# Kernel optimization log

Measured on AMD Instinct MI355X. Metric: run time of the kernel, lower is better.

## Reference

```python
import jax, jax.numpy as jnp
import numpy as np

N = 10000        # nodes
E = 160000       # edges
C = 128          # channel multiplicity (128x0e input)
RBF = 20         # edge_attr_dim
HID = 32         # edge MLP hidden
WN = 3 * C       # tp.weight_numel: 3 uvu paths (0e x Y_l -> l), 128 weights each


def setup_inputs() -> dict:
    key = jax.random.key(0)
    ks = jax.random.split(key, 12)
    f = lambda k, s, sc=1.0: jax.random.normal(k, s, jnp.float32) * sc
    return {
        "node_feat": f(ks[0], (N, C)),
        "edge_attr": f(ks[1], (E, RBF)),
        "edge_rsh": f(ks[2], (E, 9)),
        "edge_index": jax.random.randint(ks[3], (2, E), 0, N),
        # mlp_edge_scalar: Linear(2C->32), Linear(32->WN)
        "Ws1": f(ks[4], (2 * C, HID), 1.0 / np.sqrt(2 * C)), "bs1": jnp.zeros((HID,), jnp.float32),
        "Ws2": f(ks[5], (HID, WN), 1.0 / np.sqrt(HID)), "bs2": jnp.zeros((WN,), jnp.float32),
        # mlp_edge_rbf: Linear(20->32), Linear(32->WN)
        "Wr1": f(ks[6], (RBF, HID), 1.0 / np.sqrt(RBF)), "br1": jnp.zeros((HID,), jnp.float32),
        "Wr2": f(ks[7], (HID, WN), 1.0 / np.sqrt(HID)), "br2": jnp.zeros((WN,), jnp.float32),
        "lin2_w0": f(ks[8], (C, C)), "lin2_b0": jnp.zeros((C,), jnp.float32),
        "lin2_w1": f(ks[9], (C, C)),
        "lin2_w2": f(ks[10], (C, C)),
    }


def reference(node_feat, edge_attr, edge_rsh, edge_index,
              Ws1, bs1, Ws2, bs2, Wr1, br1, Wr2, br2,
              lin2_w0, lin2_b0, lin2_w1, lin2_w2):
    src, dst = edge_index[0], edge_index[1]
    xi = node_feat[src]            # [E, C] gathered scalars (center node)
    xj = node_feat[dst]            # [E, C] gathered scalars (neighbor)

    # First-layer branch: inner_dot of pure scalars -> elementwise product;
    # slice [:, C:] is empty, so s0 = concat(x_i scalars, x_j scalars).
    s0 = jnp.concatenate([xi, xj], axis=-1)  # [E, 2C]

    silu = jax.nn.silu
    w_s = silu(s0 @ Ws1 + bs1) @ Ws2 + bs2            # [E, 3C]
    w_r = silu(edge_attr @ Wr1 + br1) @ Wr2 + br2      # [E, 3C]
    tpw = w_s * w_r                                    # gated tensor-product weights

    w0, w1, w2 = tpw[:, :C], tpw[:, C:2 * C], tpw[:, 2 * C:]
    y0, y1, y2 = edge_rsh[:, :1], edge_rsh[:, 1:4], edge_rsh[:, 4:9]

    # uvu tensor product: per edge, per channel u: w_l[u] * x[u] * Y_l[m]
    m0 = (w0 * xj) * y0                                        # [E, C]
    m1 = (w1 * xj)[:, :, None] * y1[:, None, :]                # [E, C, 3]
    m2 = (w2 * xj)[:, :, None] * y2[:, None, :]                # [E, C, 5]
    msg = jnp.concatenate(
        [m0, m1.reshape(-1, 3 * C), m2.reshape(-1, 5 * C)], axis=-1)  # [E, 9C]

    # scatter-add to destination (edge_index[0])
    accu = jax.ops.segment_sum(msg, src, num_segments=node_feat.shape[0])  # [N, 9C]

    # lin_node2: equivariant linear (per-l channel mixing, bias on scalars only)
    a0 = accu[:, :C]
    a1 = accu[:, C:4 * C].reshape(-1, C, 3)
    a2 = accu[:, 4 * C:].reshape(-1, C, 5)
    inv = 1.0 / np.sqrt(C)  # e3nn o3.Linear fan-in normalization
    o0 = a0 @ lin2_w0 * inv + lin2_b0
    o1 = jnp.einsum('ncm,cd->ndm', a1, lin2_w1) * inv
    o2 = jnp.einsum('ncm,cd->ndm', a2, lin2_w2) * inv
    return jnp.concatenate([o0, o1.reshape(-1, 3 * C), o2.reshape(-1, 5 * C)], axis=-1)
```

## Files before the change

### kernel.cpp

```cpp
#include <hip/hip_runtime.h>
#include <hip/hip_bf16.h>
#include <math.h>

#define NN   10000
#define EE   160000
#define CC   128
#define RBFD 20
#define HIDD 32
#define WND  384
#define MROW 1152
#define EPB  64

typedef _Float16 half2_t __attribute__((ext_vector_type(2)));

__device__ __forceinline__ half2_t u2h(unsigned int u)
{
    union { unsigned int u; half2_t h; } c; c.u = u; return c.h;
}
__device__ __forceinline__ unsigned int pack_h2(float a, float b)
{
    union { half2_t h; unsigned int u; } c;
    c.h.x = (_Float16)a; c.h.y = (_Float16)b; return c.u;
}

__device__ __align__(16) float g_proj[(size_t)NN * 64];
__device__ __align__(16) float g_accu[(size_t)NN * MROW];
__device__ int g_deg[NN];
__device__ int g_offs[NN + 1];
__device__ int g_rel[EE];
__device__ int g_ord[EE];

__device__ __forceinline__ float silu_f(float x) { return x / (1.f + __expf(-x)); }

__global__ __launch_bounds__(256) void zero_kernel()
{
    int tid = blockIdx.x * 256 + threadIdx.x;
    if (tid < NN) g_deg[tid] = 0;
    float4* p = reinterpret_cast<float4*>(g_accu);
    float4 z = make_float4(0.f, 0.f, 0.f, 0.f);
    int n4 = NN * MROW / 4;
    for (int i = tid; i < n4; i += gridDim.x * 256) p[i] = z;
}

__global__ __launch_bounds__(256) void hist_kernel(const int* __restrict__ edge_index)
{
    int e = blockIdx.x * 256 + threadIdx.x;
    if (e < EE) g_rel[e] = atomicAdd(&g_deg[edge_index[e]], 1);
}

__global__ __launch_bounds__(256) void scan_kernel()
{
    __shared__ int sP[256];
    int t = threadIdx.x;
    int lo = t * 40, hi = min(lo + 40, NN);
    int sum = 0;
    for (int i = lo; i < hi; ++i) sum += g_deg[i];
    sP[t] = sum;
    __syncthreads();
    for (int off = 1; off < 256; off <<= 1) {
        int v = (t >= off) ? sP[t - off] : 0;
        __syncthreads();
        sP[t] += v;
        __syncthreads();
    }
    int run = sP[t] - sum;
    if (t == 0) g_offs[0] = 0;
    for (int i = lo; i < hi; ++i) { run += g_deg[i]; g_offs[i + 1] = run; }
}

__global__ __launch_bounds__(256) void proj_kernel(
    const float* __restrict__ nf,
    const float* __restrict__ Ws1, const float* __restrict__ bs1,
    const int* __restrict__ edge_index)
{
    __shared__ float sX[16][132];

    int tid = threadIdx.x;
    int nb = blockIdx.x * 16;

    {
        int eg = blockIdx.x * 256 + tid;
        g_ord[g_offs[edge_index[eg]] + g_rel[eg]] = eg;
    }

    #pragma unroll
    for (int i = tid; i < 512; i += 256) {
        int n = i >> 5, k4 = i & 31;
        float4 v = reinterpret_cast<const float4*>(nf + (size_t)(nb + n) * CC)[k4];
        sX[n][k4 * 4 + 0] = v.x;
        sX[n][k4 * 4 + 1] = v.y;
        sX[n][k4 * 4 + 2] = v.z;
        sX[n][k4 * 4 + 3] = v.w;
    }
    __syncthreads();

    int nl = tid >> 4;
    int qd = tid & 15;
    int j0 = (qd & 7) * 4;
    int rbase = (qd >= 8) ? CC : 0;

    float4 acc;
    if (qd < 8) acc = *reinterpret_cast<const float4*>(&bs1[j0]);
    else        acc = make_float4(0.f, 0.f, 0.f, 0.f);

    const float* wb = Ws1 + (size_t)rbase * HIDD + j0;
    #pragma unroll 4
    for (int k = 0; k < CC; ++k) {
        float f = sX[nl][k];
        float4 w = *reinterpret_cast<const float4*>(wb + (size_t)k * HIDD);
        acc.x = fmaf(f, w.x, acc.x);
        acc.y = fmaf(f, w.y, acc.y);
        acc.z = fmaf(f, w.z, acc.z);
        acc.w = fmaf(f, w.w, acc.w);
    }

    float* o = g_proj + (size_t)(nb + nl) * 64 + ((qd >= 8) ? HIDD : 0) + j0;
    *reinterpret_cast<float4*>(o) = acc;
}

template<int K, int YB, int MOFF>
__device__ __forceinline__ void section_pass(
    int sec, int l,
    const float2* __restrict__ nf2,
    const float* __restrict__ Ws2, const float* __restrict__ bs2,
    const float* __restrict__ Wr2, const float* __restrict__ br2,
    const unsigned int (*__restrict__ sH)[36], const float (*__restrict__ sY)[9],
    const int* __restrict__ sSrc, const int* __restrict__ sDst)
{
    unsigned int W0p[16], W1p[16], R0p[16], R1p[16];
    #pragma unroll
    for (int p = 0; p < 16; ++p) {
        int b0 = (2 * p) * WND + sec * 128 + 2 * l;
        int b1 = (2 * p + 1) * WND + sec * 128 + 2 * l;
        W0p[p] = pack_h2(Ws2[b0],     Ws2[b1]);
        W1p[p] = pack_h2(Ws2[b0 + 1], Ws2[b1 + 1]);
        R0p[p] = pack_h2(Wr2[b0],     Wr2[b1]);
        R1p[p] = pack_h2(Wr2[b0 + 1], Wr2[b1 + 1]);
    }
    #pragma unroll
    for (int p = 0; p < 16; ++p)
        asm volatile("" : "+v"(W0p[p]), "+v"(W1p[p]), "+v"(R0p[p]), "+v"(R1p[p]));

    float2 bsv = *reinterpret_cast<const float2*>(&bs2[sec * 128 + 2 * l]);
    float2 brv = *reinterpret_cast<const float2*>(&br2[sec * 128 + 2 * l]);

    float racc0[K], racc1[K];
    #pragma unroll
    for (int k = 0; k < K; ++k) { racc0[k] = 0.f; racc1[k] = 0.f; }
    int cur = sSrc[0];
    float2 xjn = nf2[(size_t)sDst[0] * 64 + l];

    #pragma unroll 2
    for (int ee = 0; ee < EPB; ++ee) {
        int src = sSrc[ee];
        if (src != cur) {
            float* ab = g_accu + (size_t)cur * MROW + MOFF + 2 * l;
            #pragma unroll
            for (int k = 0; k < K; ++k) {
                unsafeAtomicAdd(ab + k * CC,     racc0[k]);
                unsafeAtomicAdd(ab + k * CC + 1, racc1[k]);
                racc0[k] = 0.f; racc1[k] = 0.f;
            }
            cur = src;
        }
        float2 xj = xjn;
        xjn = nf2[(size_t)sDst[(ee + 1) & (EPB - 1)] * 64 + l];
        const uint4* hp = reinterpret_cast<const uint4*>(&sH[ee][0]);
        float as0 = bsv.x, as1 = bsv.y, ar0 = brv.x, ar1 = brv.y;
        #pragma unroll
        for (int q = 0; q < 4; ++q) {
            uint4 hv = hp[q];
            uint4 rv = hp[4 + q];
            as0 = __builtin_amdgcn_fdot2(u2h(hv.x), u2h(W0p[4 * q + 0]), as0, false);
            as1 = __builtin_amdgcn_fdot2(u2h(hv.x), u2h(W1p[4 * q + 0]), as1, false);
            as0 = __builtin_amdgcn_fdot2(u2h(hv.y), u2h(W0p[4 * q + 1]), as0, false);
            as1 = __builtin_amdgcn_fdot2(u2h(hv.y), u2h(W1p[4 * q + 1]), as1, false);
            as0 = __builtin_amdgcn_fdot2(u2h(hv.z), u2h(W0p[4 * q + 2]), as0, false);
            as1 = __builtin_amdgcn_fdot2(u2h(hv.z), u2h(W1p[4 * q + 2]), as1, false);
            as0 = __builtin_amdgcn_fdot2(u2h(hv.w), u2h(W0p[4 * q + 3]), as0, false);
            as1 = __builtin_amdgcn_fdot2(u2h(hv.w), u2h(W1p[4 * q + 3]), as1, false);
            ar0 = __builtin_amdgcn_fdot2(u2h(rv.x), u2h(R0p[4 * q + 0]), ar0, false);
            ar1 = __builtin_amdgcn_fdot2(u2h(rv.x), u2h(R1p[4 * q + 0]), ar1, false);
            ar0 = __builtin_amdgcn_fdot2(u2h(rv.y), u2h(R0p[4 * q + 1]), ar0, false);
            ar1 = __builtin_amdgcn_fdot2(u2h(rv.y), u2h(R1p[4 * q + 1]), ar1, false);
            ar0 = __builtin_amdgcn_fdot2(u2h(rv.z), u2h(R0p[4 * q + 2]), ar0, false);
            ar1 = __builtin_amdgcn_fdot2(u2h(rv.z), u2h(R1p[4 * q + 2]), ar1, false);
            ar0 = __builtin_amdgcn_fdot2(u2h(rv.w), u2h(R0p[4 * q + 3]), ar0, false);
            ar1 = __builtin_amdgcn_fdot2(u2h(rv.w), u2h(R1p[4 * q + 3]), ar1, false);
        }
        float u0 = as0 * ar0 * xj.x;
        float u1 = as1 * ar1 * xj.y;
        #pragma unroll
        for (int k = 0; k < K; ++k) {
            float yv = sY[ee][YB + k];
            racc0[k] = fmaf(u0, yv, racc0[k]);
            racc1[k] = fmaf(u1, yv, racc1[k]);
        }
    }
    float* ab = g_accu + (size_t)cur * MROW + MOFF + 2 * l;
    #pragma unroll
    for (int k = 0; k < K; ++k) {
        unsafeAtomicAdd(ab + k * CC,     racc0[k]);
        unsafeAtomicAdd(ab + k * CC + 1, racc1[k]);
    }
}

__global__ __launch_bounds__(192, 1) void fused_kernel(
    const float* __restrict__ nf,
    const float* __restrict__ edge_attr,
    const float* __restrict__ edge_rsh,
    const int*   __restrict__ edge_index,
    const float* __restrict__ Ws2, const float* __restrict__ bs2,
    const float* __restrict__ Wr1, const float* __restrict__ br1,
    const float* __restrict__ Wr2, const float* __restrict__ br2)
{
    __shared__ unsigned int sH[EPB][36];
    __shared__ float sY[EPB][9];
    __shared__ int   sSrc[EPB], sDst[EPB];

    int tid = threadIdx.x;
    int w = tid / 64;
    int l = tid & 63;
    int p = blockIdx.x * EPB + l;
    int e = g_ord[p];

    if (w == 0) {
        int s = edge_index[e];
        int t = edge_index[EE + e];
        const float4* pi = reinterpret_cast<const float4*>(g_proj + (size_t)s * 64);
        const float4* pj = reinterpret_cast<const float4*>(g_proj + (size_t)t * 64 + HIDD);
        #pragma unroll
        for (int j4 = 0; j4 < HIDD / 8; ++j4) {
            float4 a0 = pi[2 * j4],     b0 = pj[2 * j4];
            float4 a1 = pi[2 * j4 + 1], b1 = pj[2 * j4 + 1];
            sH[l][4 * j4 + 0] = pack_h2(silu_f(a0.x + b0.x), silu_f(a0.y + b0.y));
            sH[l][4 * j4 + 1] = pack_h2(silu_f(a0.z + b0.z), silu_f(a0.w + b0.w));
            sH[l][4 * j4 + 2] = pack_h2(silu_f(a1.x + b1.x), silu_f(a1.y + b1.y));
            sH[l][4 * j4 + 3] = pack_h2(silu_f(a1.z + b1.z), silu_f(a1.w + b1.w));
        }
        sSrc[l] = s;
        sDst[l] = t;
    } else if (w == 1) {
        float hr[HIDD];
        #pragma unroll
        for (int j = 0; j < HIDD; ++j) hr[j] = br1[j];
        #pragma unroll 1
        for (int k4 = 0; k4 < RBFD / 4; ++k4) {
            float4 a = reinterpret_cast<const float4*>(edge_attr + (size_t)e * RBFD)[k4];
            const float* wp = Wr1 + (4 * k4) * HIDD;
            #pragma unroll
            for (int j = 0; j < HIDD; ++j) {
                hr[j] = fmaf(a.x, wp[j], hr[j]);
                hr[j] = fmaf(a.y, wp[HIDD + j], hr[j]);
                hr[j] = fmaf(a.z, wp[2 * HIDD + j], hr[j]);
                hr[j] = fmaf(a.w, wp[3 * HIDD + j], hr[j]);
            }
        }
        #pragma unroll
        for (int pp = 0; pp < 16; ++pp)
            sH[l][16 + pp] = pack_h2(silu_f(hr[2 * pp]), silu_f(hr[2 * pp + 1]));
    } else {
        #pragma unroll
        for (int i = 0; i < 9; ++i) sY[l][i] = edge_rsh[(size_t)e * 9 + i];
    }
    __syncthreads();

    const float2* nf2 = reinterpret_cast<const float2*>(nf);
    if (w == 0)
        section_pass<1, 0, 0>     (0, l, nf2, Ws2, bs2, Wr2, br2, sH, sY, sSrc, sDst);
    else if (w == 1)
        section_pass<3, 1, CC>    (1, l, nf2, Ws2, bs2, Wr2, br2, sH, sY, sSrc, sDst);
    else
        section_pass<5, 4, 4 * CC>(2, l, nf2, Ws2, bs2, Wr2, br2, sH, sY, sSrc, sDst);
}

__global__ __launch_bounds__(256) void lin2_kernel(
    const float* __restrict__ W0, const float* __restrict__ b0,
    const float* __restrict__ W1, const float* __restrict__ W2,
    float* __restrict__ out)
{
    __shared__ float sA[8 * MROW];
    int n0 = blockIdx.x * 8;
    const float4* g = reinterpret_cast<const float4*>(g_accu + (size_t)n0 * MROW);
    for (int i = threadIdx.x; i < 8 * MROW / 4; i += 256)
        reinterpret_cast<float4*>(sA)[i] = g[i];
    __syncthreads();

    int d  = threadIdx.x & (CC - 1);
    int nl = threadIdx.x >> 7;

    float acc[4][9];
    #pragma unroll
    for (int q = 0; q < 4; ++q)
        #pragma unroll
        for (int m = 0; m < 9; ++m) acc[q][m] = 0.f;

    #pragma unroll 1
    for (int c = 0; c < CC; ++c) {
        float w0 = W0[c * CC + d];
        float w1 = W1[c * CC + d];
        float w2 = W2[c * CC + d];
        #pragma unroll
        for (int q = 0; q < 4; ++q) {
            const float* a = sA + (size_t)(nl * 4 + q) * MROW;
            acc[q][0] = fmaf(a[c],          w0, acc[q][0]);
            acc[q][1] = fmaf(a[CC + c],     w1, acc[q][1]);
            acc[q][2] = fmaf(a[2 * CC + c], w1, acc[q][2]);
            acc[q][3] = fmaf(a[3 * CC + c], w1, acc[q][3]);
            acc[q][4] = fmaf(a[4 * CC + c], w2, acc[q][4]);
            acc[q][5] = fmaf(a[5 * CC + c], w2, acc[q][5]);
            acc[q][6] = fmaf(a[6 * CC + c], w2, acc[q][6]);
            acc[q][7] = fmaf(a[7 * CC + c], w2, acc[q][7]);
            acc[q][8] = fmaf(a[8 * CC + c], w2, acc[q][8]);
        }
    }

    const float inv = 0.08838834764831845f;
    #pragma unroll
    for (int q = 0; q < 4; ++q) {
        size_t ob = (size_t)(n0 + nl * 4 + q) * MROW;
        out[ob + d] = acc[q][0] * inv + b0[d];
        #pragma unroll
        for (int m = 0; m < 3; ++m) out[ob + CC + d * 3 + m]     = acc[q][1 + m] * inv;
        #pragma unroll
        for (int m = 0; m < 5; ++m) out[ob + 4 * CC + d * 5 + m] = acc[q][4 + m] * inv;
    }
}

extern "C" void kernel_launch(void* const* d_in, const int* in_sizes, int n_in,
                              void* d_out, int out_size, void* d_ws, size_t ws_size,
                              hipStream_t stream)
{
    const float* node_feat  = (const float*)d_in[0];
    const float* edge_attr  = (const float*)d_in[1];
    const float* edge_rsh   = (const float*)d_in[2];
    const int*   edge_index = (const int*)  d_in[3];
    const float* Ws1 = (const float*)d_in[4];
    const float* bs1 = (const float*)d_in[5];
    const float* Ws2 = (const float*)d_in[6];
    const float* bs2 = (const float*)d_in[7];
    const float* Wr1 = (const float*)d_in[8];
    const float* br1 = (const float*)d_in[9];
    const float* Wr2 = (const float*)d_in[10];
    const float* br2 = (const float*)d_in[11];
    const float* W0  = (const float*)d_in[12];
    const float* b0  = (const float*)d_in[13];
    const float* W1  = (const float*)d_in[14];
    const float* W2  = (const float*)d_in[15];
    float* out = (float*)d_out;

    zero_kernel<<<2048, 256, 0, stream>>>();
    hist_kernel<<<EE / 256, 256, 0, stream>>>(edge_index);
    scan_kernel<<<1, 256, 0, stream>>>();
    proj_kernel<<<NN / 16, 256, 0, stream>>>(node_feat, Ws1, bs1, edge_index);
    fused_kernel<<<EE / EPB, 192, 0, stream>>>(
        node_feat, edge_attr, edge_rsh, edge_index,
        Ws2, bs2, Wr1, br1, Wr2, br2);
    lin2_kernel<<<NN / 8, 256, 0, stream>>>(W0, b0, W1, W2, out);
}
```

Before: 284.3 us.

## Prepack fp16 MLP weights in a separate kernel and raise fused-kernel occupancy

A new single-block pack_kernel converts the Ws2/Wr2 second-layer weights to packed half2 once per call and stores them in a global buffer in a coalesced uint4 layout. Each wave of the fused kernel then loads its 16 uint4 weight registers directly, instead of doing 128 strided fp32 loads plus conversions per block. The launch bound goes from 1 to 4 blocks per SIMD to hide memory and atomic latency, at the risk of register pressure and spills. It also adds one small kernel launch.

```diff
diff --git a/kernel.cpp b/kernel.cpp
--- a/kernel.cpp
+++ b/kernel.cpp
@@ -25,6 +25,7 @@
 
 __device__ __align__(16) float g_proj[(size_t)NN * 64];
 __device__ __align__(16) float g_accu[(size_t)NN * MROW];
+__device__ __align__(16) uint4 g_wp[3 * 16 * 64];
 __device__ int g_deg[NN];
 __device__ int g_offs[NN + 1];
 __device__ int g_rel[EE];
@@ -40,6 +41,32 @@
     float4 z = make_float4(0.f, 0.f, 0.f, 0.f);
     int n4 = NN * MROW / 4;
     for (int i = tid; i < n4; i += gridDim.x * 256) p[i] = z;
+}
+
+__global__ __launch_bounds__(192) void pack_kernel(
+    const float* __restrict__ Ws2, const float* __restrict__ Wr2)
+{
+    int tid = threadIdx.x;
+    int sec = tid >> 6, l = tid & 63;
+    int c0 = sec * 128 + 2 * l;
+    #pragma unroll
+    for (int q = 0; q < 4; ++q) {
+        unsigned int w0[4], w1[4], r0[4], r1[4];
+        #pragma unroll
+        for (int i = 0; i < 4; ++i) {
+            int p = 4 * q + i;
+            int b0 = (2 * p) * WND + c0;
+            int b1 = (2 * p + 1) * WND + c0;
+            w0[i] = pack_h2(Ws2[b0],     Ws2[b1]);
+            w1[i] = pack_h2(Ws2[b0 + 1], Ws2[b1 + 1]);
+            r0[i] = pack_h2(Wr2[b0],     Wr2[b1]);
+            r1[i] = pack_h2(Wr2[b0 + 1], Wr2[b1 + 1]);
+        }
+        g_wp[((sec * 16 + 0 * 4 + q) * 64) + l] = make_uint4(w0[0], w0[1], w0[2], w0[3]);
+        g_wp[((sec * 16 + 1 * 4 + q) * 64) + l] = make_uint4(w1[0], w1[1], w1[2], w1[3]);
+        g_wp[((sec * 16 + 2 * 4 + q) * 64) + l] = make_uint4(r0[0], r0[1], r0[2], r0[3]);
+        g_wp[((sec * 16 + 3 * 4 + q) * 64) + l] = make_uint4(r1[0], r1[1], r1[2], r1[3]);
+    }
 }
 
 __global__ __launch_bounds__(256) void hist_kernel(const int* __restrict__ edge_index)
@@ -122,24 +149,19 @@
 __device__ __forceinline__ void section_pass(
     int sec, int l,
     const float2* __restrict__ nf2,
-    const float* __restrict__ Ws2, const float* __restrict__ bs2,
-    const float* __restrict__ Wr2, const float* __restrict__ br2,
+    const float* __restrict__ bs2, const float* __restrict__ br2,
     const unsigned int (*__restrict__ sH)[36], const float (*__restrict__ sY)[9],
     const int* __restrict__ sSrc, const int* __restrict__ sDst)
 {
-    unsigned int W0p[16], W1p[16], R0p[16], R1p[16];
-    #pragma unroll
-    for (int p = 0; p < 16; ++p) {
-        int b0 = (2 * p) * WND + sec * 128 + 2 * l;
-        int b1 = (2 * p + 1) * WND + sec * 128 + 2 * l;
-        W0p[p] = pack_h2(Ws2[b0],     Ws2[b1]);
-        W1p[p] = pack_h2(Ws2[b0 + 1], Ws2[b1 + 1]);
-        R0p[p] = pack_h2(Wr2[b0],     Wr2[b1]);
-        R1p[p] = pack_h2(Wr2[b0 + 1], Wr2[b1 + 1]);
-    }
-    #pragma unroll
-    for (int p = 0; p < 16; ++p)
-        asm volatile("" : "+v"(W0p[p]), "+v"(W1p[p]), "+v"(R0p[p]), "+v"(R1p[p]));
+    const uint4* wt = g_wp + (size_t)sec * 16 * 64 + l;
+    uint4 W0q[4], W1q[4], R0q[4], R1q[4];
+    #pragma unroll
+    for (int q = 0; q < 4; ++q) {
+        W0q[q] = wt[(0 * 4 + q) * 64];
+        W1q[q] = wt[(1 * 4 + q) * 64];
+        R0q[q] = wt[(2 * 4 + q) * 64];
+        R1q[q] = wt[(3 * 4 + q) * 64];
+    }
 
     float2 bsv = *reinterpret_cast<const float2*>(&bs2[sec * 128 + 2 * l]);
     float2 brv = *reinterpret_cast<const float2*>(&br2[sec * 128 + 2 * l]);
@@ -171,22 +193,22 @@
         for (int q = 0; q < 4; ++q) {
             uint4 hv = hp[q];
             uint4 rv = hp[4 + q];
-            as0 = __builtin_amdgcn_fdot2(u2h(hv.x), u2h(W0p[4 * q + 0]), as0, false);
-            as1 = __builtin_amdgcn_fdot2(u2h(hv.x), u2h(W1p[4 * q + 0]), as1, false);
-            as0 = __builtin_amdgcn_fdot2(u2h(hv.y), u2h(W0p[4 * q + 1]), as0, false);
-            as1 = __builtin_amdgcn_fdot2(u2h(hv.y), u2h(W1p[4 * q + 1]), as1, false);
-            as0 = __builtin_amdgcn_fdot2(u2h(hv.z), u2h(W0p[4 * q + 2]), as0, false);
-            as1 = __builtin_amdgcn_fdot2(u2h(hv.z), u2h(W1p[4 * q + 2]), as1, false);
-            as0 = __builtin_amdgcn_fdot2(u2h(hv.w), u2h(W0p[4 * q + 3]), as0, false);
-            as1 = __builtin_amdgcn_fdot2(u2h(hv.w), u2h(W1p[4 * q + 3]), as1, false);
-            ar0 = __builtin_amdgcn_fdot2(u2h(rv.x), u2h(R0p[4 * q + 0]), ar0, false);
-            ar1 = __builtin_amdgcn_fdot2(u2h(rv.x), u2h(R1p[4 * q + 0]), ar1, false);
-            ar0 = __builtin_amdgcn_fdot2(u2h(rv.y), u2h(R0p[4 * q + 1]), ar0, false);
-            ar1 = __builtin_amdgcn_fdot2(u2h(rv.y), u2h(R1p[4 * q + 1]), ar1, false);
-            ar0 = __builtin_amdgcn_fdot2(u2h(rv.z), u2h(R0p[4 * q + 2]), ar0, false);
-            ar1 = __builtin_amdgcn_fdot2(u2h(rv.z), u2h(R1p[4 * q + 2]), ar1, false);
-            ar0 = __builtin_amdgcn_fdot2(u2h(rv.w), u2h(R0p[4 * q + 3]), ar0, false);
-            ar1 = __builtin_amdgcn_fdot2(u2h(rv.w), u2h(R1p[4 * q + 3]), ar1, false);
+            as0 = __builtin_amdgcn_fdot2(u2h(hv.x), u2h(W0q[q].x), as0, false);
+            as1 = __builtin_amdgcn_fdot2(u2h(hv.x), u2h(W1q[q].x), as1, false);
+            as0 = __builtin_amdgcn_fdot2(u2h(hv.y), u2h(W0q[q].y), as0, false);
+            as1 = __builtin_amdgcn_fdot2(u2h(hv.y), u2h(W1q[q].y), as1, false);
+            as0 = __builtin_amdgcn_fdot2(u2h(hv.z), u2h(W0q[q].z), as0, false);
+            as1 = __builtin_amdgcn_fdot2(u2h(hv.z), u2h(W1q[q].z), as1, false);
+            as0 = __builtin_amdgcn_fdot2(u2h(hv.w), u2h(W0q[q].w), as0, false);
+            as1 = __builtin_amdgcn_fdot2(u2h(hv.w), u2h(W1q[q].w), as1, false);
+            ar0 = __builtin_amdgcn_fdot2(u2h(rv.x), u2h(R0q[q].x), ar0, false);
+            ar1 = __builtin_amdgcn_fdot2(u2h(rv.x), u2h(R1q[q].x), ar1, false);
+            ar0 = __builtin_amdgcn_fdot2(u2h(rv.y), u2h(R0q[q].y), ar0, false);
+            ar1 = __builtin_amdgcn_fdot2(u2h(rv.y), u2h(R1q[q].y), ar1, false);
+            ar0 = __builtin_amdgcn_fdot2(u2h(rv.z), u2h(R0q[q].z), ar0, false);
+            ar1 = __builtin_amdgcn_fdot2(u2h(rv.z), u2h(R1q[q].z), ar1, false);
+            ar0 = __builtin_amdgcn_fdot2(u2h(rv.w), u2h(R0q[q].w), ar0, false);
+            ar1 = __builtin_amdgcn_fdot2(u2h(rv.w), u2h(R1q[q].w), ar1, false);
         }
         float u0 = as0 * ar0 * xj.x;
         float u1 = as1 * ar1 * xj.y;
@@ -205,14 +227,14 @@
     }
 }
 
-__global__ __launch_bounds__(192, 1) void fused_kernel(
+__global__ __launch_bounds__(192, 4) void fused_kernel(
     const float* __restrict__ nf,
     const float* __restrict__ edge_attr,
     const float* __restrict__ edge_rsh,
     const int*   __restrict__ edge_index,
-    const float* __restrict__ Ws2, const float* __restrict__ bs2,
+    const float* __restrict__ bs2,
     const float* __restrict__ Wr1, const float* __restrict__ br1,
-    const float* __restrict__ Wr2, const float* __restrict__ br2)
+    const float* __restrict__ br2)
 {
     __shared__ unsigned int sH[EPB][36];
     __shared__ float sY[EPB][9];
@@ -267,11 +289,11 @@
 
     const float2* nf2 = reinterpret_cast<const float2*>(nf);
     if (w == 0)
-        section_pass<1, 0, 0>     (0, l, nf2, Ws2, bs2, Wr2, br2, sH, sY, sSrc, sDst);
+        section_pass<1, 0, 0>     (0, l, nf2, bs2, br2, sH, sY, sSrc, sDst);
     else if (w == 1)
-        section_pass<3, 1, CC>    (1, l, nf2, Ws2, bs2, Wr2, br2, sH, sY, sSrc, sDst);
+        section_pass<3, 1, CC>    (1, l, nf2, bs2, br2, sH, sY, sSrc, sDst);
     else
-        section_pass<5, 4, 4 * CC>(2, l, nf2, Ws2, bs2, Wr2, br2, sH, sY, sSrc, sDst);
+        section_pass<5, 4, 4 * CC>(2, l, nf2, bs2, br2, sH, sY, sSrc, sDst);
 }
 
 __global__ __launch_bounds__(256) void lin2_kernel(
@@ -350,11 +372,12 @@
     float* out = (float*)d_out;
 
     zero_kernel<<<2048, 256, 0, stream>>>();
+    pack_kernel<<<1, 192, 0, stream>>>(Ws2, Wr2);
     hist_kernel<<<EE / 256, 256, 0, stream>>>(edge_index);
     scan_kernel<<<1, 256, 0, stream>>>();
     proj_kernel<<<NN / 16, 256, 0, stream>>>(node_feat, Ws1, bs1, edge_index);
     fused_kernel<<<EE / EPB, 192, 0, stream>>>(
         node_feat, edge_attr, edge_rsh, edge_index,
-        Ws2, bs2, Wr1, br1, Wr2, br2);
+        bs2, Wr1, br1, br2);
     lin2_kernel<<<NN / 8, 256, 0, stream>>>(W0, b0, W1, W2, out);
 }
```

Result: no change. 283.7 us (-0.2%).
